# Kernel optimization log

Measured on AMD Instinct MI355X. Metric: run time of the kernel, lower is better.

Reference implementation:

```python
import jax, jax.numpy as jnp
import numpy as np

PS = 32
D = 256


def setup_inputs() -> dict:
    key = jax.random.key(0)
    ks = jax.random.split(key, 9)
    B, L = 32, 32768
    s_in = 1.0 / np.sqrt(PS)
    s_d = 1.0 / np.sqrt(D)
    return {
        "x": jax.random.normal(ks[0], (B, L), dtype=jnp.float32),
        "W_proj": jax.random.normal(ks[1], (PS, D), dtype=jnp.float32) * s_in,
        "b_proj": jnp.zeros((D,), jnp.float32),
        "W_qkv": jax.random.normal(ks[2], (D, 3 * D), dtype=jnp.float32) * s_d,
        "b_qkv": jnp.zeros((3 * D,), jnp.float32),
        "W_out": jax.random.normal(ks[3], (D, D), dtype=jnp.float32) * s_d,
        "b_out": jnp.zeros((D,), jnp.float32),
        "W_head": jax.random.normal(ks[4], (D, PS), dtype=jnp.float32) * s_d,
        "b_head": jnp.zeros((PS,), jnp.float32),
    }


def reference(x, W_proj, b_proj, W_qkv, b_qkv, W_out, b_out, W_head, b_head):
    B, L = x.shape
    T = L // PS
    # InstanceNorm over full series (torch .std is unbiased -> ddof=1)
    mean = jnp.mean(x, axis=-1, keepdims=True)
    std = jnp.std(x, axis=-1, keepdims=True, ddof=1) + 1e-5
    x_norm = (x - mean) / std
    patches = x_norm.reshape(B, T, PS)
    # Patch embedding
    h = patches @ W_proj + b_proj  # [B, T, D]
    # Single-head causal self-attention (explicit scores, as in source)
    qkv = h @ W_qkv + b_qkv
    q, k, v = jnp.split(qkv, 3, axis=-1)
    scale = 1.0 / jnp.sqrt(jnp.asarray(D, dtype=h.dtype))
    attn = jnp.einsum("btd,bsd->bts", q, k) * scale  # [B, T, T]
    causal = jnp.tril(jnp.ones((T, T), dtype=bool))
    attn = jnp.where(causal, attn, -jnp.inf)
    attn = jax.nn.softmax(attn, axis=-1)
    out = jnp.einsum("bts,bsd->btd", attn, v)
    out = out @ W_out + b_out
    # Prediction head + next-patch MSE loss
    pred = out @ W_head + b_head  # [B, T, PS]
    loss = jnp.mean((pred[:, :-1] - patches[:, 1:]) ** 2)
    return loss
```

## Files before the change

### kernel.cpp

```cpp
#include <hip/hip_runtime.h>
#include <math.h>

#define B_SZ 32
#define L_SZ 32768
#define T_SZ 1024
#define PS_SZ 32
#define D_SZ 256
#define SM_M 10.0f

typedef float f32x4 __attribute__((ext_vector_type(4)));
typedef short s16x8 __attribute__((ext_vector_type(8)));
typedef unsigned short u16x8 __attribute__((ext_vector_type(8)));

__device__ __forceinline__ unsigned short f2bf(float f) {
  union { float f; unsigned int u; } v; v.f = f;
  unsigned int r = v.u + 0x7FFFu + ((v.u >> 16) & 1u);
  return (unsigned short)(r >> 16);
}

__device__ __forceinline__ void g2l16(const unsigned short* g, unsigned short* l) {
  __builtin_amdgcn_global_load_lds(
      (const __attribute__((address_space(1))) unsigned int*)g,
      (__attribute__((address_space(3))) unsigned int*)l, 16, 0, 0);
}

__global__ __launch_bounds__(256) void prep_kernel(const float* __restrict__ x,
                                                   float* __restrict__ sgpart,
                                                   const float* __restrict__ Wp,
                                                   const float* __restrict__ bp,
                                                   const float* __restrict__ Wq,
                                                   const float* __restrict__ bq,
                                                   const float* __restrict__ Wo,
                                                   const float* __restrict__ bo,
                                                   const float* __restrict__ Wh,
                                                   const float* __restrict__ bh,
                                                   float* __restrict__ Wcb,
                                                   unsigned short* __restrict__ WqT,
                                                   unsigned short* __restrict__ WfT,
                                                   float* __restrict__ bfp,
                                                   unsigned int* __restrict__ total,
                                                   float* __restrict__ lsum) {
  __shared__ float red[8];
  const int g = blockIdx.x, tid = threadIdx.x;
  const int w = tid >> 6, lane = tid & 63;
  if (g < 256) {
    const int b = g >> 3;
    const float* p = x + (size_t)b * L_SZ + (size_t)(g & 7) * 4096;
    float s = 0.f, ss = 0.f;
#pragma unroll
    for (int i = 0; i < 4; ++i) {
      float4 f = ((const float4*)p)[tid + i * 256];
      s += f.x + f.y + f.z + f.w;
      ss += f.x * f.x + f.y * f.y + f.z * f.z + f.w * f.w;
    }
#pragma unroll
    for (int off = 32; off >= 1; off >>= 1) {
      s += __shfl_down(s, off);
      ss += __shfl_down(ss, off);
    }
    if (lane == 0) { red[w] = s; red[4 + w] = ss; }
    __syncthreads();
    if (tid == 0) {
      sgpart[g * 2]     = red[0] + red[1] + red[2] + red[3];
      sgpart[g * 2 + 1] = red[4] + red[5] + red[6] + red[7];
    }
  } else if (g < 388) {
    int idx = (g - 256) * 256 + tid;
    if (idx < 33 * 768) {
      int p = idx / 768, j = idx % 768;
      const float* arow = (p < 32) ? (Wp + p * 256) : bp;
      float acc = (p < 32) ? 0.f : bq[j];
      for (int d = 0; d < 256; ++d) acc += arow[d] * Wq[d * 768 + j];
      if (p < 32) WqT[j * 32 + p] = f2bf(acc);
      else Wcb[j] = acc;
    } else {
      int k = idx - 33 * 768;
      if (k < 8192) {
        int p = k >> 8, d = k & 255;
        float acc = 0.f;
        for (int e = 0; e < 256; ++e) acc += Wo[d * 256 + e] * Wh[e * 32 + p];
        WfT[p * 256 + d] = f2bf(acc);
      } else if (k < 8224) {
        int p = k - 8192;
        float acc = bh[p];
        for (int e = 0; e < 256; ++e) acc += bo[e] * Wh[e * 32 + p];
        bfp[p] = acc;
      }
    }
  } else {
    if (tid == 0) { total[0] = 0u; lsum[0] = 0.f; }
  }
}

__global__ __launch_bounds__(256) void qkv_kernel(const float* __restrict__ x,
                                                  const float* __restrict__ sgpart,
                                                  const unsigned short* __restrict__ WqT,
                                                  const float* __restrict__ Wcb,
                                                  unsigned short* __restrict__ Qb,
                                                  unsigned short* __restrict__ Kb,
                                                  unsigned short* __restrict__ Vtt) {
  __shared__ unsigned short T4[4][8448];
  const int tid = threadIdx.x;
  const int w = tid >> 6, lane = tid & 63;
  const int lo = lane & 15, quad = lane >> 4;
  unsigned short* Tw = T4[w];
  const int mbase = blockIdx.x * 128 + w * 32;
  const int b = mbase >> 10;
  float S = 0.f, SS = 0.f;
#pragma unroll
  for (int i = 0; i < 8; ++i) {
    S += sgpart[(b * 8 + i) * 2];
    SS += sgpart[(b * 8 + i) * 2 + 1];
  }
  const float mean = S * (1.f / (float)L_SZ);
  const float var = (SS - S * mean) * (1.f / (float)(L_SZ - 1));
  const float inv = 1.f / (sqrtf(var) + 1e-5f);
  s16x8 af0, af1;
  {
    float4 a = *(const float4*)&x[(size_t)(mbase + lo) * 32 + quad * 8];
    float4 c = *(const float4*)&x[(size_t)(mbase + lo) * 32 + quad * 8 + 4];
    af0[0] = (short)f2bf((a.x - mean) * inv); af0[1] = (short)f2bf((a.y - mean) * inv);
    af0[2] = (short)f2bf((a.z - mean) * inv); af0[3] = (short)f2bf((a.w - mean) * inv);
    af0[4] = (short)f2bf((c.x - mean) * inv); af0[5] = (short)f2bf((c.y - mean) * inv);
    af0[6] = (short)f2bf((c.z - mean) * inv); af0[7] = (short)f2bf((c.w - mean) * inv);
    float4 d = *(const float4*)&x[(size_t)(mbase + 16 + lo) * 32 + quad * 8];
    float4 e = *(const float4*)&x[(size_t)(mbase + 16 + lo) * 32 + quad * 8 + 4];
    af1[0] = (short)f2bf((d.x - mean) * inv); af1[1] = (short)f2bf((d.y - mean) * inv);
    af1[2] = (short)f2bf((d.z - mean) * inv); af1[3] = (short)f2bf((d.w - mean) * inv);
    af1[4] = (short)f2bf((e.x - mean) * inv); af1[5] = (short)f2bf((e.y - mean) * inv);
    af1[6] = (short)f2bf((e.z - mean) * inv); af1[7] = (short)f2bf((e.w - mean) * inv);
  }
#pragma unroll 4
  for (int nt = 0; nt < 16; ++nt) {
    s16x8 bf = *(const s16x8*)&WqT[(size_t)(nt * 16 + lo) * 32 + quad * 8];
    f32x4 c0 = {0.f, 0.f, 0.f, 0.f}, c1 = {0.f, 0.f, 0.f, 0.f};
    c0 = __builtin_amdgcn_mfma_f32_16x16x32_bf16(af0, bf, c0, 0, 0, 0);
    c1 = __builtin_amdgcn_mfma_f32_16x16x32_bf16(af1, bf, c1, 0, 0, 0);
    const int col = nt * 16 + lo;
    const float bi = Wcb[col];
#pragma unroll
    for (int i = 0; i < 4; ++i) {
      Tw[(quad * 4 + i) * 264 + col]      = f2bf((c0[i] + bi) * 0.0625f);
      Tw[(16 + quad * 4 + i) * 264 + col] = f2bf((c1[i] + bi) * 0.0625f);
    }
  }
#pragma unroll
  for (int it = 0; it < 16; ++it) {
    const int gsub = it * 64 + lane;
    const int row = gsub >> 5, c16 = gsub & 31;
    *(u16x8*)&Qb[(size_t)(mbase + row) * 256 + c16 * 8] =
        *(const u16x8*)&Tw[row * 264 + c16 * 8];
  }
#pragma unroll 4
  for (int nt = 0; nt < 16; ++nt) {
    s16x8 bf = *(const s16x8*)&WqT[(size_t)(256 + nt * 16 + lo) * 32 + quad * 8];
    f32x4 c0 = {0.f, 0.f, 0.f, 0.f}, c1 = {0.f, 0.f, 0.f, 0.f};
    c0 = __builtin_amdgcn_mfma_f32_16x16x32_bf16(af0, bf, c0, 0, 0, 0);
    c1 = __builtin_amdgcn_mfma_f32_16x16x32_bf16(af1, bf, c1, 0, 0, 0);
    const int col = nt * 16 + lo;
    const float bi = Wcb[256 + col];
#pragma unroll
    for (int i = 0; i < 4; ++i) {
      Tw[(quad * 4 + i) * 264 + col]      = f2bf(c0[i] + bi);
      Tw[(16 + quad * 4 + i) * 264 + col] = f2bf(c1[i] + bi);
    }
  }
#pragma unroll
  for (int it = 0; it < 16; ++it) {
    const int gsub = it * 64 + lane;
    const int row = gsub >> 5, c16 = gsub & 31;
    *(u16x8*)&Kb[(size_t)(mbase + row) * 256 + c16 * 8] =
        *(const u16x8*)&Tw[row * 264 + c16 * 8];
  }
#pragma unroll 4
  for (int nt2 = 0; nt2 < 16; ++nt2) {
    s16x8 aw = *(const s16x8*)&WqT[(size_t)(512 + nt2 * 16 + lo) * 32 + quad * 8];
    f32x4 c0 = {0.f, 0.f, 0.f, 0.f}, c1 = {0.f, 0.f, 0.f, 0.f};
    c0 = __builtin_amdgcn_mfma_f32_16x16x32_bf16(aw, af0, c0, 0, 0, 0);
    c1 = __builtin_amdgcn_mfma_f32_16x16x32_bf16(aw, af1, c1, 0, 0, 0);
#pragma unroll
    for (int i = 0; i < 4; ++i) {
      const int d = nt2 * 16 + quad * 4 + i;
      const float bv = Wcb[512 + d];
      Tw[d * 32 + lo]      = f2bf(c0[i] + bv);
      Tw[d * 32 + 16 + lo] = f2bf(c1[i] + bv);
    }
  }
  {
    const int ktq = (mbase >> 5) & 31;
    const size_t vb = ((size_t)b * 32 + ktq) * 8192;
#pragma unroll
    for (int it = 0; it < 16; ++it) {
      const int gsub = it * 64 + lane;
      *(u16x8*)&Vtt[vb + gsub * 8] = *(const u16x8*)&Tw[gsub * 8];
    }
  }
}

__global__ __launch_bounds__(256) void attn_kernel(const unsigned short* __restrict__ Qb,
                                                   const unsigned short* __restrict__ Kb,
                                                   const unsigned short* __restrict__ Vtt,
                                                   const unsigned short* __restrict__ WfT,
                                                   const float* __restrict__ bfp,
                                                   const float* __restrict__ x,
                                                   const float* __restrict__ sgpart,
                                                   float* __restrict__ lsum,
                                                   unsigned int* __restrict__ total,
                                                   float* __restrict__ out) {
  __shared__ unsigned short SMEM[39040];
  const int g = blockIdx.x;
  const int b = (g & 7) * 4 + ((g >> 3) & 3);
  const int qt = 7 - (g >> 5);
  const int tid = threadIdx.x;
  const int w = tid >> 6, lane = tid & 63;
  const int lo = lane & 15, quad = lane >> 4;

  const int qr0 = qt * 128 + w * 32;
  const size_t kbase = (size_t)b << 10;

  s16x8 qf[2][8];
#pragma unroll
  for (int mt = 0; mt < 2; ++mt) {
    const size_t qrow = (kbase + qr0 + mt * 16 + lo) * 256;
#pragma unroll
    for (int kc = 0; kc < 8; ++kc)
      qf[mt][kc] = *(const s16x8*)&Qb[qrow + kc * 32 + quad * 8];
  }

  f32x4 O[2][16];
#pragma unroll
  for (int mt = 0; mt < 2; ++mt)
#pragma unroll
    for (int nt = 0; nt < 16; ++nt) O[mt][nt] = (f32x4){0.f, 0.f, 0.f, 0.f};
  f32x4 Ol[2] = {{0.f, 0.f, 0.f, 0.f}, {0.f, 0.f, 0.f, 0.f}};
  s16x8 ones;
#pragma unroll
  for (int jj = 0; jj < 8; ++jj) ones[jj] = (short)0x3F80;

  const int c16p = tid & 31;
  const int keyr = tid >> 5;
  const int c16s = (c16p & 24) | ((c16p & 7) ^ keyr);
  const unsigned short* kgp = Kb + (kbase << 8) + keyr * 256 + c16s * 8;
  const int dql = tid >> 2;
  const int cpq = (tid & 3) ^ ((tid >> 3) & 3);
  const unsigned short* vgp = Vtt + (size_t)b * 262144 + dql * 32 + cpq * 8;
  const int ldst = (w * 64) * 8;

  unsigned short* myp = &SMEM[32768 + w * 1280];
  const int lo7 = lo & 7;
  const int nk = 4 * qt + 4;

#pragma unroll
  for (int it = 0; it < 4; ++it) g2l16(kgp + it * 2048, &SMEM[it * 2048 + ldst]);
#pragma unroll
  for (int it = 0; it < 4; ++it) g2l16(vgp + it * 2048, &SMEM[8192 + it * 2048 + ldst]);
  kgp += 8192; vgp += 8192;

  for (int kt = 0; kt < nk; ++kt) {
    const int k0 = kt * 32;
    __syncthreads();
    const int cur = (kt & 1) << 14;
    if (kt + 1 < nk) {
      const int nxt = ((kt + 1) & 1) << 14;
#pragma unroll
      for (int it = 0; it < 4; ++it) g2l16(kgp + it * 2048, &SMEM[nxt + it * 2048 + ldst]);
#pragma unroll
      for (int it = 0; it < 4; ++it)
        g2l16(vgp + it * 2048, &SMEM[nxt + 8192 + it * 2048 + ldst]);
      kgp += 8192; vgp += 8192;
    }

    if (k0 <= qr0 + 31) {
      f32x4 s[2][2];
#pragma unroll
      for (int mt = 0; mt < 2; ++mt)
#pragma unroll
        for (int nt = 0; nt < 2; ++nt) s[mt][nt] = (f32x4){0.f, 0.f, 0.f, 0.f};
#pragma unroll
      for (int kc = 0; kc < 8; ++kc) {
        const int c16 = kc * 4 + quad;
        const int cs = (c16 & 24) | ((c16 & 7) ^ lo7);
        s16x8 kf0 = *(const s16x8*)&SMEM[cur + (lo * 32 + cs) * 8];
        s16x8 kf1 = *(const s16x8*)&SMEM[cur + ((16 + lo) * 32 + cs) * 8];
        s[0][0] = __builtin_amdgcn_mfma_f32_16x16x32_bf16(qf[0][kc], kf0, s[0][0], 0, 0, 0);
        s[0][1] = __builtin_amdgcn_mfma_f32_16x16x32_bf16(qf[0][kc], kf1, s[0][1], 0, 0, 0);
        s[1][0] = __builtin_amdgcn_mfma_f32_16x16x32_bf16(qf[1][kc], kf0, s[1][0], 0, 0, 0);
        s[1][1] = __builtin_amdgcn_mfma_f32_16x16x32_bf16(qf[1][kc], kf1, s[1][1], 0, 0, 0);
      }
      if (k0 + 31 > qr0) {
#pragma unroll
        for (int mt = 0; mt < 2; ++mt)
#pragma unroll
          for (int ii = 0; ii < 4; ++ii) {
            const int row = qr0 + mt * 16 + quad * 4 + ii;
            if (k0 + lo > row) s[mt][0][ii] = -1e30f;
            if (k0 + 16 + lo > row) s[mt][1][ii] = -1e30f;
          }
      }
#pragma unroll
      for (int mt = 0; mt < 2; ++mt)
#pragma unroll
        for (int ii = 0; ii < 4; ++ii) {
          myp[(mt * 16 + quad * 4 + ii) * 40 + lo]      = f2bf(__expf(s[mt][0][ii] - SM_M));
          myp[(mt * 16 + quad * 4 + ii) * 40 + 16 + lo] = f2bf(__expf(s[mt][1][ii] - SM_M));
        }
      s16x8 pf0 = *(const s16x8*)&myp[lo * 40 + quad * 8];
      s16x8 pf1 = *(const s16x8*)&myp[(16 + lo) * 40 + quad * 8];
      Ol[0] = __builtin_amdgcn_mfma_f32_16x16x32_bf16(pf0, ones, Ol[0], 0, 0, 0);
      Ol[1] = __builtin_amdgcn_mfma_f32_16x16x32_bf16(pf1, ones, Ol[1], 0, 0, 0);
#pragma unroll
      for (int nt = 0; nt < 16; ++nt) {
        const int d = nt * 16 + lo;
        const int cp = quad ^ ((d >> 1) & 3);
        s16x8 vf = *(const s16x8*)&SMEM[cur + 8192 + ((d << 2) + cp) * 8];
        O[0][nt] = __builtin_amdgcn_mfma_f32_16x16x32_bf16(pf0, vf, O[0][nt], 0, 0, 0);
        O[1][nt] = __builtin_amdgcn_mfma_f32_16x16x32_bf16(pf1, vf, O[1][nt], 0, 0, 0);
      }
    }
  }
  __syncthreads();

  unsigned short* OLw = &SMEM[w * 8448];
#pragma unroll
  for (int mt = 0; mt < 2; ++mt) {
    float inv4[4];
#pragma unroll
    for (int ii = 0; ii < 4; ++ii) inv4[ii] = 1.f / Ol[mt][ii];
#pragma unroll
    for (int nt = 0; nt < 16; ++nt)
#pragma unroll
      for (int ii = 0; ii < 4; ++ii)
        OLw[(mt * 16 + quad * 4 + ii) * 264 + nt * 16 + lo] = f2bf(O[mt][nt][ii] * inv4[ii]);
  }

  s16x8 af[2][8];
#pragma unroll
  for (int kc = 0; kc < 8; ++kc) {
    af[0][kc] = *(const s16x8*)&OLw[lo * 264 + kc * 32 + quad * 8];
    af[1][kc] = *(const s16x8*)&OLw[(16 + lo) * 264 + kc * 32 + quad * 8];
  }

  float S = 0.f, SS = 0.f;
#pragma unroll
  for (int i = 0; i < 8; ++i) {
    S += sgpart[(b * 8 + i) * 2];
    SS += sgpart[(b * 8 + i) * 2 + 1];
  }
  const float mean = S * (1.f / (float)L_SZ);
  const float var = (SS - S * mean) * (1.f / (float)(L_SZ - 1));
  const float invb = 1.f / (sqrtf(var) + 1e-5f);

  float lacc = 0.f;
#pragma unroll
  for (int nt = 0; nt < 2; ++nt) {
    f32x4 acc0 = {0.f, 0.f, 0.f, 0.f}, acc1 = {0.f, 0.f, 0.f, 0.f};
#pragma unroll
    for (int kc = 0; kc < 8; ++kc) {
      s16x8 bfr = *(const s16x8*)&WfT[(size_t)(nt * 16 + lo) * 256 + kc * 32 + quad * 8];
      acc0 = __builtin_amdgcn_mfma_f32_16x16x32_bf16(af[0][kc], bfr, acc0, 0, 0, 0);
      acc1 = __builtin_amdgcn_mfma_f32_16x16x32_bf16(af[1][kc], bfr, acc1, 0, 0, 0);
    }
    const float ba = bfp[nt * 16 + lo];
    const int p = nt * 16 + lo;
#pragma unroll
    for (int ii = 0; ii < 4; ++ii) {
      const int t0 = qr0 + quad * 4 + ii;
      if (t0 < 1023) {
        const float pr = acc0[ii] + ba;
        const float tg = (x[(size_t)b * L_SZ + (t0 + 1) * 32 + p] - mean) * invb;
        const float d = pr - tg;
        lacc += d * d;
      }
      const int t1 = qr0 + 16 + quad * 4 + ii;
      if (t1 < 1023) {
        const float pr = acc1[ii] + ba;
        const float tg = (x[(size_t)b * L_SZ + (t1 + 1) * 32 + p] - mean) * invb;
        const float d = pr - tg;
        lacc += d * d;
      }
    }
  }
#pragma unroll
  for (int off = 32; off >= 1; off >>= 1) lacc += __shfl_down(lacc, off);
  float* redf = (float*)&SMEM[38912];
  unsigned int* flag = (unsigned int*)&SMEM[38960];
  if (lane == 0) redf[w] = lacc;
  __syncthreads();

  if (tid == 0) {
    atomicAdd(lsum, redf[0] + redf[1] + redf[2] + redf[3]);
    __threadfence();
    unsigned int prev = atomicAdd(total, 1u);
    flag[0] = (prev == 255u) ? 1u : 0u;
  }
  __syncthreads();
  if (flag[0] && tid == 0) {
    float tot = atomicAdd(lsum, 0.0f);
    out[0] = tot * (1.f / (float)(B_SZ * (T_SZ - 1) * PS_SZ));
  }
}

extern "C" void kernel_launch(void* const* d_in, const int* in_sizes, int n_in,
                              void* d_out, int out_size, void* d_ws, size_t ws_size,
                              hipStream_t stream) {
  const float* x      = (const float*)d_in[0];
  const float* W_proj = (const float*)d_in[1];
  const float* b_proj = (const float*)d_in[2];
  const float* W_qkv  = (const float*)d_in[3];
  const float* b_qkv  = (const float*)d_in[4];
  const float* W_out  = (const float*)d_in[5];
  const float* b_out  = (const float*)d_in[6];
  const float* W_head = (const float*)d_in[7];
  const float* b_head = (const float*)d_in[8];
  float* out = (float*)d_out;
  char* ws = (char*)d_ws;

  unsigned short* Qb     = (unsigned short*)ws;
  unsigned short* Kb     = (unsigned short*)(ws + (16ull << 20));
  unsigned short* Vtt    = (unsigned short*)(ws + (32ull << 20));
  char* tail = ws + (48ull << 20);
  float*          Wcb    = (float*)tail;
  unsigned short* WqT    = (unsigned short*)(tail + 4096);
  unsigned short* WfT    = (unsigned short*)(tail + 65536);
  float*          bfp    = (float*)(tail + 98304);
  float*          sgpart = (float*)(tail + 102400);
  unsigned int*   total  = (unsigned int*)(tail + 106496);
  float*          lsum   = (float*)(tail + 106496 + 64);

  prep_kernel<<<389, 256, 0, stream>>>(x, sgpart, W_proj, b_proj, W_qkv, b_qkv,
                                       W_out, b_out, W_head, b_head,
                                       Wcb, WqT, WfT, bfp, total, lsum);
  qkv_kernel<<<256, 256, 0, stream>>>(x, sgpart, WqT, Wcb, Qb, Kb, Vtt);
  attn_kernel<<<256, 256, 0, stream>>>(Qb, Kb, Vtt, WfT, bfp, x, sgpart, lsum, total, out);
}
```

Measured before the change: 184.5 us.

## Halve attention block to two waves, double grid, drop K/V double buffering

The attention kernel now uses 128-thread blocks covering 64 query rows each, launched as 512 blocks instead of 256. The shared-memory footprint shrinks to one K/V tile buffer, loaded synchronously each iteration with an extra barrier instead of prefetched into a double buffer. The intent is better occupancy and load balance across CUs for the causal workload. In exchange, each K/V tile is reused by fewer query rows, global traffic rises, and load latency is no longer overlapped with compute.

Result: slower. 190.3 us (+3.2%).

```diff
diff --git a/kernel.cpp b/kernel.cpp
--- a/kernel.cpp
+++ b/kernel.cpp
@@ -197,7 +197,7 @@
   }
 }
 
-__global__ __launch_bounds__(256) void attn_kernel(const unsigned short* __restrict__ Qb,
+__global__ __launch_bounds__(128) void attn_kernel(const unsigned short* __restrict__ Qb,
                                                    const unsigned short* __restrict__ Kb,
                                                    const unsigned short* __restrict__ Vtt,
                                                    const unsigned short* __restrict__ WfT,
@@ -207,15 +207,15 @@
                                                    float* __restrict__ lsum,
                                                    unsigned int* __restrict__ total,
                                                    float* __restrict__ out) {
-  __shared__ unsigned short SMEM[39040];
+  __shared__ unsigned short SMEM[18944];
   const int g = blockIdx.x;
   const int b = (g & 7) * 4 + ((g >> 3) & 3);
-  const int qt = 7 - (g >> 5);
+  const int qt = 15 - (g >> 5);
   const int tid = threadIdx.x;
   const int w = tid >> 6, lane = tid & 63;
   const int lo = lane & 15, quad = lane >> 4;
 
-  const int qr0 = qt * 128 + w * 32;
+  const int qr0 = qt * 64 + w * 32;
   const size_t kbase = (size_t)b << 10;
 
   s16x8 qf[2][8];
@@ -237,38 +237,31 @@
 #pragma unroll
   for (int jj = 0; jj < 8; ++jj) ones[jj] = (short)0x3F80;
 
+  const int k5 = tid >> 5;
   const int c16p = tid & 31;
-  const int keyr = tid >> 5;
-  const int c16s = (c16p & 24) | ((c16p & 7) ^ keyr);
-  const unsigned short* kgp = Kb + (kbase << 8) + keyr * 256 + c16s * 8;
-  const int dql = tid >> 2;
+  const int c16sA = (c16p & 24) | ((c16p & 7) ^ k5);
+  const int c16sB = c16sA ^ 4;
+  const unsigned short* kgpA = Kb + (kbase << 8) + k5 * 256 + c16sA * 8;
+  const unsigned short* kgpB = Kb + (kbase << 8) + (4 + k5) * 256 + c16sB * 8;
   const int cpq = (tid & 3) ^ ((tid >> 3) & 3);
-  const unsigned short* vgp = Vtt + (size_t)b * 262144 + dql * 32 + cpq * 8;
-  const int ldst = (w * 64) * 8;
-
-  unsigned short* myp = &SMEM[32768 + w * 1280];
+  const unsigned short* vgp = Vtt + (size_t)b * 262144 + (tid >> 2) * 32 + cpq * 8;
+
+  unsigned short* myp = &SMEM[16384 + w * 1280];
   const int lo7 = lo & 7;
-  const int nk = 4 * qt + 4;
-
-#pragma unroll
-  for (int it = 0; it < 4; ++it) g2l16(kgp + it * 2048, &SMEM[it * 2048 + ldst]);
-#pragma unroll
-  for (int it = 0; it < 4; ++it) g2l16(vgp + it * 2048, &SMEM[8192 + it * 2048 + ldst]);
-  kgp += 8192; vgp += 8192;
+  const int nk = 2 * (qt + 1);
 
   for (int kt = 0; kt < nk; ++kt) {
     const int k0 = kt * 32;
     __syncthreads();
-    const int cur = (kt & 1) << 14;
-    if (kt + 1 < nk) {
-      const int nxt = ((kt + 1) & 1) << 14;
-#pragma unroll
-      for (int it = 0; it < 4; ++it) g2l16(kgp + it * 2048, &SMEM[nxt + it * 2048 + ldst]);
-#pragma unroll
-      for (int it = 0; it < 4; ++it)
-        g2l16(vgp + it * 2048, &SMEM[nxt + 8192 + it * 2048 + ldst]);
-      kgp += 8192; vgp += 8192;
-    }
+#pragma unroll
+    for (int it2 = 0; it2 < 4; ++it2) {
+      g2l16(kgpA + (size_t)kt * 8192 + it2 * 2048, &SMEM[(it2 * 256 + w * 64) * 8]);
+      g2l16(kgpB + (size_t)kt * 8192 + it2 * 2048, &SMEM[((it2 * 256 + 128) + w * 64) * 8]);
+    }
+#pragma unroll
+    for (int it = 0; it < 8; ++it)
+      g2l16(vgp + (size_t)kt * 8192 + it * 1024, &SMEM[8192 + (it * 128 + w * 64) * 8]);
+    __syncthreads();
 
     if (k0 <= qr0 + 31) {
       f32x4 s[2][2];
@@ -280,8 +273,8 @@
       for (int kc = 0; kc < 8; ++kc) {
         const int c16 = kc * 4 + quad;
         const int cs = (c16 & 24) | ((c16 & 7) ^ lo7);
-        s16x8 kf0 = *(const s16x8*)&SMEM[cur + (lo * 32 + cs) * 8];
-        s16x8 kf1 = *(const s16x8*)&SMEM[cur + ((16 + lo) * 32 + cs) * 8];
+        s16x8 kf0 = *(const s16x8*)&SMEM[(lo * 32 + cs) * 8];
+        s16x8 kf1 = *(const s16x8*)&SMEM[((16 + lo) * 32 + cs) * 8];
         s[0][0] = __builtin_amdgcn_mfma_f32_16x16x32_bf16(qf[0][kc], kf0, s[0][0], 0, 0, 0);
         s[0][1] = __builtin_amdgcn_mfma_f32_16x16x32_bf16(qf[0][kc], kf1, s[0][1], 0, 0, 0);
         s[1][0] = __builtin_amdgcn_mfma_f32_16x16x32_bf16(qf[1][kc], kf0, s[1][0], 0, 0, 0);
@@ -312,7 +305,7 @@
       for (int nt = 0; nt < 16; ++nt) {
         const int d = nt * 16 + lo;
         const int cp = quad ^ ((d >> 1) & 3);
-        s16x8 vf = *(const s16x8*)&SMEM[cur + 8192 + ((d << 2) + cp) * 8];
+        s16x8 vf = *(const s16x8*)&SMEM[8192 + ((d << 2) + cp) * 8];
         O[0][nt] = __builtin_amdgcn_mfma_f32_16x16x32_bf16(pf0, vf, O[0][nt], 0, 0, 0);
         O[1][nt] = __builtin_amdgcn_mfma_f32_16x16x32_bf16(pf1, vf, O[1][nt], 0, 0, 0);
       }
@@ -382,16 +375,16 @@
   }
 #pragma unroll
   for (int off = 32; off >= 1; off >>= 1) lacc += __shfl_down(lacc, off);
-  float* redf = (float*)&SMEM[38912];
-  unsigned int* flag = (unsigned int*)&SMEM[38960];
+  float* redf = (float*)&SMEM[17024];
+  unsigned int* flag = (unsigned int*)&SMEM[17120];
   if (lane == 0) redf[w] = lacc;
   __syncthreads();
 
   if (tid == 0) {
-    atomicAdd(lsum, redf[0] + redf[1] + redf[2] + redf[3]);
+    atomicAdd(lsum, redf[0] + redf[1]);
     __threadfence();
     unsigned int prev = atomicAdd(total, 1u);
-    flag[0] = (prev == 255u) ? 1u : 0u;
+    flag[0] = (prev == 511u) ? 1u : 0u;
   }
   __syncthreads();
   if (flag[0] && tid == 0) {
@@ -431,5 +424,5 @@
                                        W_out, b_out, W_head, b_head,
                                        Wcb, WqT, WfT, bfp, total, lsum);
   qkv_kernel<<<256, 256, 0, stream>>>(x, sgpart, WqT, Wcb, Qb, Kb, Vtt);
-  attn_kernel<<<256, 256, 0, stream>>>(Qb, Kb, Vtt, WfT, bfp, x, sgpart, lsum, total, out);
-}
+  attn_kernel<<<512, 128, 0, stream>>>(Qb, Kb, Vtt, WfT, bfp, x, sgpart, lsum, total, out);
+}
```
